# Optimization experiments

Measured on AMD Instinct MI355X. Metric: run time of the kernel, lower is better.

The kernel has to match this reference:

```python
import jax, jax.numpy as jnp
import numpy as np

NUM_PITCHES = 88
H_FEAT = 188
LSTM_UNITS = 48
N_STATES = 5
CTX_HID = 16
CTX_OUT = 4


def _glorot(key, shape):
    fan_in, fan_out = shape[1], shape[0]
    lim = (6.0 / (fan_in + fan_out)) ** 0.5
    return jax.random.uniform(key, shape, jnp.float32, -lim, lim)


def setup_inputs() -> dict:
    key = jax.random.key(0)
    ks = jax.random.split(key, 16)
    B, T = 16, 256
    pitch_features = jax.random.normal(ks[0], (B, NUM_PITCHES, H_FEAT, T), jnp.float32)
    prev_context = jax.random.uniform(ks[1], (B, NUM_PITCHES, 3), jnp.float32)
    # context net params
    fc1_w = _glorot(ks[2], (CTX_HID, 3)); fc1_b = jnp.zeros((CTX_HID,), jnp.float32)
    fc2_w = _glorot(ks[3], (CTX_HID, CTX_HID)); fc2_b = jnp.zeros((CTX_HID,), jnp.float32)
    fc3_w = _glorot(ks[4], (CTX_OUT, CTX_HID)); fc3_b = jnp.zeros((CTX_OUT,), jnp.float32)
    # lstm1: input H_FEAT+4 -> 48; gates order i,f,g,o (torch convention)
    in1 = H_FEAT + CTX_OUT
    lstm1_wih = _glorot(ks[5], (4 * LSTM_UNITS, in1))
    lstm1_whh = _glorot(ks[6], (4 * LSTM_UNITS, LSTM_UNITS))
    lstm1_bih = jnp.zeros((4 * LSTM_UNITS,), jnp.float32)
    lstm1_bhh = jnp.zeros((4 * LSTM_UNITS,), jnp.float32)
    lstm2_wih = _glorot(ks[7], (4 * LSTM_UNITS, LSTM_UNITS))
    lstm2_whh = _glorot(ks[8], (4 * LSTM_UNITS, LSTM_UNITS))
    lstm2_bih = jnp.zeros((4 * LSTM_UNITS,), jnp.float32)
    lstm2_bhh = jnp.zeros((4 * LSTM_UNITS,), jnp.float32)
    fc_states_w = _glorot(ks[9], (N_STATES, LSTM_UNITS))
    fc_states_b = jnp.zeros((N_STATES,), jnp.float32)
    return dict(pitch_features=pitch_features, prev_context=prev_context,
                fc1_w=fc1_w, fc1_b=fc1_b, fc2_w=fc2_w, fc2_b=fc2_b,
                fc3_w=fc3_w, fc3_b=fc3_b,
                lstm1_wih=lstm1_wih, lstm1_whh=lstm1_whh, lstm1_bih=lstm1_bih, lstm1_bhh=lstm1_bhh,
                lstm2_wih=lstm2_wih, lstm2_whh=lstm2_whh, lstm2_bih=lstm2_bih, lstm2_bhh=lstm2_bhh,
                fc_states_w=fc_states_w, fc_states_b=fc_states_b)


def _lstm_scan(x, wih, whh, bih, bhh):
    # x: (S, N, In); zero init state; returns (S, N, U)
    S, N, _ = x.shape
    U = whh.shape[1]
    xg = jnp.einsum('sni,gi->sng', x, wih) + bih + bhh  # precompute input gates

    def step(carry, xg_t):
        h, c = carry
        g = xg_t + h @ whh.T  # (N, 4U)
        i, f, gg, o = jnp.split(g, 4, axis=-1)
        c = jax.nn.sigmoid(f) * c + jax.nn.sigmoid(i) * jnp.tanh(gg)
        h = jax.nn.sigmoid(o) * jnp.tanh(c)
        return (h, c), h

    init = (jnp.zeros((N, U), x.dtype), jnp.zeros((N, U), x.dtype))
    _, hs = jax.lax.scan(step, init, xg)
    return hs


def reference(pitch_features, prev_context,
              fc1_w, fc1_b, fc2_w, fc2_b, fc3_w, fc3_b,
              lstm1_wih, lstm1_whh, lstm1_bih, lstm1_bhh,
              lstm2_wih, lstm2_whh, lstm2_bih, lstm2_bhh,
              fc_states_w, fc_states_b):
    B, P, H, T = pitch_features.shape
    # Context net (context never updates across t in the original loop)
    x = jax.nn.relu(prev_context @ fc1_w.T + fc1_b)
    x = jax.nn.relu(x @ fc2_w.T + fc2_b)
    ctx_emb = x @ fc3_w.T + fc3_b  # (B, P, 4)
    # Each timestep t is independent: LSTM runs over the pitch axis (len 88)
    # with zero initial state every step. Fold (B, T) into batch N.
    pf = jnp.transpose(pitch_features, (1, 0, 3, 2)).reshape(P, B * T, H)  # (P, BT, H)
    ce = jnp.broadcast_to(ctx_emb[:, None, :, :], (B, T, P, CTX_OUT))
    ce = jnp.transpose(ce, (2, 0, 1, 3)).reshape(P, B * T, CTX_OUT)
    seq = jnp.concatenate([pf, ce], axis=-1)  # (P, BT, H+4)
    h = _lstm_scan(seq, lstm1_wih, lstm1_whh, lstm1_bih, lstm1_bhh)
    h = _lstm_scan(h, lstm2_wih, lstm2_whh, lstm2_bih, lstm2_bhh)
    logits = h @ fc_states_w.T + fc_states_b  # (P, BT, 5)
    logits = logits.reshape(P, B, T, N_STATES)
    logits = jnp.transpose(logits, (1, 0, 3, 2))  # (B, P, 5, T)
    return jax.nn.softmax(logits, axis=2)
```

## Files before the change

### kernel.cpp

```cpp
#include <hip/hip_runtime.h>
#include <hip/hip_bf16.h>
#include <cstdint>

#define P_ 88
#define B_ 16
#define T_ 256
#define H_ 188
#define G_ 192
#define U_ 48
#define N_ 4096

typedef __attribute__((ext_vector_type(8))) short bf16x8;
typedef __attribute__((ext_vector_type(8))) _Float16 f16x8;
typedef __attribute__((ext_vector_type(4))) float f32x4;

__device__ __forceinline__ float sigf(float x) {
  return __builtin_amdgcn_rcpf(1.0f + __expf(-x));
}
__device__ __forceinline__ float tanh_f(float x) {
  return 1.0f - 2.0f * __builtin_amdgcn_rcpf(1.0f + __expf(2.0f * x));
}
__device__ __forceinline__ unsigned short f2bs(float v) {
  union { __hip_bfloat16 h; unsigned short s; } u;
  u.h = __float2bfloat16(v);
  return u.s;
}
__device__ __forceinline__ float bs2f(unsigned short s) {
  union { unsigned int u; float f; } x;
  x.u = ((unsigned int)s) << 16;
  return x.f;
}
__device__ __forceinline__ float hs2f(unsigned short s) {
  union { unsigned short u; _Float16 h; } x;
  x.u = s;
  return (float)x.h;
}
__device__ __forceinline__ unsigned short f2hs(float v) {
  union { _Float16 h; unsigned short s; } x;
  x.h = (_Float16)v;
  return x.s;
}

__global__ void ctx_kernel(const float* __restrict__ pc,
                           const float* __restrict__ fc1w, const float* __restrict__ fc1b,
                           const float* __restrict__ fc2w, const float* __restrict__ fc2b,
                           const float* __restrict__ fc3w, const float* __restrict__ fc3b,
                           const float* __restrict__ wih1,
                           const float* __restrict__ bih1, const float* __restrict__ bhh1,
                           float* __restrict__ ctxg) {
  int bp = blockIdx.x * 64 + threadIdx.x;
  if (bp >= B_ * P_) return;
  float p0 = pc[bp * 3 + 0], p1 = pc[bp * 3 + 1], p2 = pc[bp * 3 + 2];
  float x1[16], x2[16];
#pragma unroll
  for (int jj = 0; jj < 16; ++jj)
    x1[jj] = fmaxf(0.f, fc1w[jj * 3 + 0] * p0 + fc1w[jj * 3 + 1] * p1 + fc1w[jj * 3 + 2] * p2 + fc1b[jj]);
#pragma unroll
  for (int jj = 0; jj < 16; ++jj) {
    float s = fc2b[jj];
#pragma unroll
    for (int i = 0; i < 16; ++i) s += fc2w[jj * 16 + i] * x1[i];
    x2[jj] = fmaxf(0.f, s);
  }
  float ce[4];
#pragma unroll
  for (int jj = 0; jj < 4; ++jj) {
    float s = fc3b[jj];
#pragma unroll
    for (int i = 0; i < 16; ++i) s += fc3w[jj * 16 + i] * x2[i];
    ce[jj] = s;
  }
  float* op = ctxg + (size_t)bp * G_;
  for (int g = 0; g < G_; ++g) {
    const float* wr = wih1 + (size_t)g * G_ + H_;
    op[g] = bih1[g] + bhh1[g] + ce[0] * wr[0] + ce[1] * wr[1] + ce[2] * wr[2] + ce[3] * wr[3];
  }
}

__global__ __launch_bounds__(256) void wfrag_kernel(const float* __restrict__ wih1,
                                                    f16x8* __restrict__ wfrag) {
  const int idx = blockIdx.x * 256 + threadIdx.x;
  if (idx >= 12 * 6 * 64) return;
  const int l = idx & 63;
  const int kc = (idx >> 6) % 6;
  const int j = idx / 384;
  const int g = j * 16 + (l & 15);
  const int k0 = kc * 32 + (l >> 4) * 8;
  f16x8 v;
#pragma unroll
  for (int e = 0; e < 8; ++e) {
    const int k = k0 + e;
    const float wv = (k < H_) ? wih1[(size_t)g * G_ + k] : 0.f;
    v[e] = (_Float16)wv;
  }
  wfrag[idx] = v;
}

__global__ __launch_bounds__(256, 3) void gemm_mfma(const float* __restrict__ pf,
                                                    const f16x8* __restrict__ wfrag,
                                                    const float* __restrict__ ctxg,
                                                    unsigned short* __restrict__ xg2) {
  const int bp = blockIdx.x >> 1, tb = blockIdx.x & 1;
  const int p = bp % P_, b = bp / P_;
  const int tid = threadIdx.x;
  const int w = tid >> 6, l = tid & 63;
  const int lj = l & 15, lq = l >> 4;

  __shared__ __align__(16) char ldsraw[49152];
  _Float16(*Ahi)[34] = (_Float16(*)[34])ldsraw;
  _Float16(*Alo)[34] = (_Float16(*)[34])(ldsraw + 8704);

  float cg[12];
#pragma unroll
  for (int jn = 0; jn < 12; ++jn)
    cg[jn] = ctxg[(size_t)bp * G_ + jn * 16 + lj];

  f32x4 acc[2][12];
#pragma unroll
  for (int mt = 0; mt < 2; ++mt)
#pragma unroll
    for (int jn = 0; jn < 12; ++jn)
#pragma unroll
      for (int r = 0; r < 4; ++r) acc[mt][jn][r] = 0.f;

  const float* Ab = pf + (size_t)bp * H_ * T_ + tb * 128;
  const int kl = tid >> 5;
  const int t4 = (tid & 31) * 4;

  for (int kc = 0; kc < 6; ++kc) {
    __syncthreads();
#pragma unroll
    for (int rr = 0; rr < 4; ++rr) {
      const int kk = rr * 8 + kl;
      const int kg = kc * 32 + kk;
      float a0 = 0.f, a1 = 0.f, a2 = 0.f, a3 = 0.f;
      if (kg < H_) {
        const float4 v = *(const float4*)(Ab + (size_t)kg * T_ + t4);
        a0 = v.x; a1 = v.y; a2 = v.z; a3 = v.w;
      }
      const _Float16 h0 = (_Float16)a0, h1 = (_Float16)a1;
      const _Float16 h2 = (_Float16)a2, h3 = (_Float16)a3;
      Ahi[t4 + 0][kk] = h0; Alo[t4 + 0][kk] = (_Float16)(a0 - (float)h0);
      Ahi[t4 + 1][kk] = h1; Alo[t4 + 1][kk] = (_Float16)(a1 - (float)h1);
      Ahi[t4 + 2][kk] = h2; Alo[t4 + 2][kk] = (_Float16)(a2 - (float)h2);
      Ahi[t4 + 3][kk] = h3; Alo[t4 + 3][kk] = (_Float16)(a3 - (float)h3);
    }
    __syncthreads();
    const int trow = w * 32;
    const f16x8 ahi0 = *(const f16x8*)&Ahi[trow + lj][lq * 8];
    const f16x8 ahi1 = *(const f16x8*)&Ahi[trow + 16 + lj][lq * 8];
    const f16x8 alo0 = *(const f16x8*)&Alo[trow + lj][lq * 8];
    const f16x8 alo1 = *(const f16x8*)&Alo[trow + 16 + lj][lq * 8];
#pragma unroll
    for (int jn = 0; jn < 12; ++jn) {
      const f16x8 wf = wfrag[(jn * 6 + kc) * 64 + l];
      acc[0][jn] = __builtin_amdgcn_mfma_f32_16x16x32_f16(ahi0, wf, acc[0][jn], 0, 0, 0);
      acc[1][jn] = __builtin_amdgcn_mfma_f32_16x16x32_f16(ahi1, wf, acc[1][jn], 0, 0, 0);
      acc[0][jn] = __builtin_amdgcn_mfma_f32_16x16x32_f16(alo0, wf, acc[0][jn], 0, 0, 0);
      acc[1][jn] = __builtin_amdgcn_mfma_f32_16x16x32_f16(alo1, wf, acc[1][jn], 0, 0, 0);
    }
  }
  __syncthreads();

  unsigned short* Cst = (unsigned short*)ldsraw + w * 6144;
#pragma unroll
  for (int mt = 0; mt < 2; ++mt)
#pragma unroll
    for (int jn = 0; jn < 12; ++jn)
#pragma unroll
      for (int r = 0; r < 4; ++r)
        Cst[mt * 3072 + jn * 256 + r * 64 + l] = f2hs(acc[mt][jn][r] + cg[jn]);
  const int nb0 = b * 16 + tb * 8 + w * 2;
  unsigned short* gb = xg2 + ((size_t)p * 256 + nb0) * 3072;
#pragma unroll
  for (int rr = 0; rr < 12; ++rr) {
    const uint4 v = *(const uint4*)(Cst + rr * 512 + l * 8);
    *(uint4*)(gb + rr * 512 + l * 8) = v;
  }
}

__global__ __launch_bounds__(256, 2) void scan_mfma(
    const unsigned short* __restrict__ xg2,
    const float* __restrict__ whh1, const float* __restrict__ wih2,
    const float* __restrict__ whh2, const float* __restrict__ bih2,
    const float* __restrict__ bhh2, const float* __restrict__ fcw,
    const float* __restrict__ fcb, float* __restrict__ out) {
  __shared__ __align__(16) short hh[16][104];
  __shared__ __align__(16) short hl[16][104];
  __shared__ __align__(16) float gs[8][196];
  __shared__ __align__(16) float h2f[8][52];
  __shared__ __align__(16) float fcws[5 * 48];
  __shared__ float logit_s[5][8];
  __shared__ float prob_s[5][8];

  const int tid = threadIdx.x;
  const int w = tid >> 6;
  const int l = tid & 63;
  const int lj = l & 15;
  const int lq = l >> 4;
  const int grp = blockIdx.x >> 1;
  const int half = blockIdx.x & 1;
  const int n0 = blockIdx.x * 8;
  const int b = n0 >> 8, t0 = n0 & 255;

  bf16x8 b1[3][2];
  bf16x8 b2f[3][3];
  float bias2r[3];
#pragma unroll
  for (int i = 0; i < 3; ++i) {
    const int j = w * 48 + i * 16 + lj;
    bias2r[i] = bih2[j] + bhh2[j];
#pragma unroll
    for (int kc = 0; kc < 2; ++kc)
#pragma unroll
      for (int e = 0; e < 8; ++e) {
        const int u = kc * 32 + lq * 8 + e;
        b1[i][kc][e] = (u < U_) ? (short)f2bs(whh1[j * U_ + u]) : (short)0;
      }
#pragma unroll
    for (int kc = 0; kc < 3; ++kc)
#pragma unroll
      for (int e = 0; e < 8; ++e) {
        const int u = kc * 32 + lq * 8 + e;
        b2f[i][kc][e] = (u < U_) ? (short)f2bs(wih2[j * U_ + u])
                                 : (short)f2bs(whh2[j * U_ + (u - U_)]);
      }
  }

  for (int e = tid; e < 16 * 104 / 2; e += 256) {
    ((unsigned int*)hh)[e] = 0u;
    ((unsigned int*)hl)[e] = 0u;
  }
  for (int e = tid; e < 5 * U_; e += 256) fcws[e] = fcw[e];

  const int tn0 = tid / U_, tu0 = tid % U_;
  const int tn1 = (256 + tid) / U_, tu1 = (256 + tid) % U_;
  float c1r[2] = {0.f, 0.f}, c2r[2] = {0.f, 0.f};
  const bool fcth = tid < 40;
  const int fk = tid >> 3, fn = tid & 7;
  const float fcbr = fcth ? fcb[fk] : 0.f;
  const int sk = (tid - 96) >> 3, sn = (tid - 96) & 7;

  unsigned short xp[12];
  {
    const size_t pb = (size_t)grp * 3072;
#pragma unroll
    for (int i = 0; i < 3; ++i)
#pragma unroll
      for (int r = 0; r < 4; ++r)
        xp[i * 4 + r] = (lq < 2)
            ? xg2[pb + (size_t)((w * 3 + i) * 256 + r * 64 + (half * 2 + lq) * 16 + lj)]
            : (unsigned short)0;
  }
  const short* hhrow = &hh[lj][0];
  const short* hlrow = &hl[lj][0];
  __syncthreads();

  for (int p = 0; p < P_; ++p) {
    f32x4 c1f[3];
#pragma unroll
    for (int i = 0; i < 3; ++i)
#pragma unroll
      for (int r = 0; r < 4; ++r) c1f[i][r] = hs2f(xp[i * 4 + r]);
    {
      bf16x8 ah0 = *(const bf16x8*)(hhrow + lq * 8);
      bf16x8 ah1 = *(const bf16x8*)(hhrow + 32 + lq * 8);
      bf16x8 al0 = *(const bf16x8*)(hlrow + lq * 8);
      bf16x8 al1 = *(const bf16x8*)(hlrow + 32 + lq * 8);
#pragma unroll
      for (int i = 0; i < 3; ++i)
        c1f[i] = __builtin_amdgcn_mfma_f32_16x16x32_bf16(ah0, b1[i][0], c1f[i], 0, 0, 0);
#pragma unroll
      for (int i = 0; i < 3; ++i)
        c1f[i] = __builtin_amdgcn_mfma_f32_16x16x32_bf16(ah1, b1[i][1], c1f[i], 0, 0, 0);
#pragma unroll
      for (int i = 0; i < 3; ++i)
        c1f[i] = __builtin_amdgcn_mfma_f32_16x16x32_bf16(al0, b1[i][0], c1f[i], 0, 0, 0);
#pragma unroll
      for (int i = 0; i < 3; ++i)
        c1f[i] = __builtin_amdgcn_mfma_f32_16x16x32_bf16(al1, b1[i][1], c1f[i], 0, 0, 0);
    }
    if (lq < 2) {
#pragma unroll
      for (int i = 0; i < 3; ++i)
#pragma unroll
        for (int r = 0; r < 4; ++r)
          gs[lq * 4 + r][w * 48 + i * 16 + lj] = c1f[i][r];
    }
    if (p > 0 && fcth) {
      float a = fcbr;
#pragma unroll
      for (int uq = 0; uq < 12; ++uq) {
        f32x4 hv = *(const f32x4*)&h2f[fn][uq * 4];
        f32x4 wv = *(const f32x4*)&fcws[fk * 48 + uq * 4];
        a += hv[0] * wv[0] + hv[1] * wv[1] + hv[2] * wv[2] + hv[3] * wv[3];
      }
      logit_s[fk][fn] = a;
    }
    __syncthreads();
    {
      const int n = tn0, u = tu0;
      const float ig = gs[n][u], fg = gs[n][48 + u];
      const float gg = gs[n][96 + u], og = gs[n][144 + u];
      const float cc = sigf(fg) * c1r[0] + sigf(ig) * tanh_f(gg);
      c1r[0] = cc;
      const float h = sigf(og) * tanh_f(cc);
      const unsigned short hb = f2bs(h);
      hh[n][u] = (short)hb;
      hl[n][u] = (short)f2bs(h - bs2f(hb));
    }
    if (tid < 128) {
      const int n = tn1, u = tu1;
      const float ig = gs[n][u], fg = gs[n][48 + u];
      const float gg = gs[n][96 + u], og = gs[n][144 + u];
      const float cc = sigf(fg) * c1r[1] + sigf(ig) * tanh_f(gg);
      c1r[1] = cc;
      const float h = sigf(og) * tanh_f(cc);
      const unsigned short hb = f2bs(h);
      hh[n][u] = (short)hb;
      hl[n][u] = (short)f2bs(h - bs2f(hb));
    }
    if (p > 0 && tid >= 192 && tid < 200) {
      const int n = tid - 192;
      const float l0 = logit_s[0][n], l1 = logit_s[1][n], l2 = logit_s[2][n],
                  l3 = logit_s[3][n], l4 = logit_s[4][n];
      const float m = fmaxf(fmaxf(fmaxf(l0, l1), fmaxf(l2, l3)), l4);
      const float e0 = __expf(l0 - m), e1 = __expf(l1 - m), e2 = __expf(l2 - m),
                  e3 = __expf(l3 - m), e4 = __expf(l4 - m);
      const float rs = __builtin_amdgcn_rcpf(e0 + e1 + e2 + e3 + e4);
      prob_s[0][n] = e0 * rs; prob_s[1][n] = e1 * rs; prob_s[2][n] = e2 * rs;
      prob_s[3][n] = e3 * rs; prob_s[4][n] = e4 * rs;
    }
    __syncthreads();
    if (p < P_ - 1) {
      const size_t pb = (size_t)((p + 1) * 256 + grp) * 3072;
#pragma unroll
      for (int i = 0; i < 3; ++i)
#pragma unroll
        for (int r = 0; r < 4; ++r)
          xp[i * 4 + r] = (lq < 2)
              ? xg2[pb + (size_t)((w * 3 + i) * 256 + r * 64 + (half * 2 + lq) * 16 + lj)]
              : (unsigned short)0;
    }
    f32x4 c2f[3];
#pragma unroll
    for (int i = 0; i < 3; ++i) {
      c2f[i][0] = bias2r[i]; c2f[i][1] = bias2r[i];
      c2f[i][2] = bias2r[i]; c2f[i][3] = bias2r[i];
    }
    {
      bf16x8 a0 = *(const bf16x8*)(hhrow + lq * 8);
      bf16x8 a1 = *(const bf16x8*)(hhrow + 32 + lq * 8);
      bf16x8 a2 = *(const bf16x8*)(hhrow + 64 + lq * 8);
      bf16x8 q0 = *(const bf16x8*)(hlrow + lq * 8);
      bf16x8 q1 = *(const bf16x8*)(hlrow + 32 + lq * 8);
      bf16x8 q2 = *(const bf16x8*)(hlrow + 64 + lq * 8);
#pragma unroll
      for (int i = 0; i < 3; ++i)
        c2f[i] = __builtin_amdgcn_mfma_f32_16x16x32_bf16(a0, b2f[i][0], c2f[i], 0, 0, 0);
#pragma unroll
      for (int i = 0; i < 3; ++i)
        c2f[i] = __builtin_amdgcn_mfma_f32_16x16x32_bf16(a1, b2f[i][1], c2f[i], 0, 0, 0);
#pragma unroll
      for (int i = 0; i < 3; ++i)
        c2f[i] = __builtin_amdgcn_mfma_f32_16x16x32_bf16(a2, b2f[i][2], c2f[i], 0, 0, 0);
#pragma unroll
      for (int i = 0; i < 3; ++i)
        c2f[i] = __builtin_amdgcn_mfma_f32_16x16x32_bf16(q0, b2f[i][0], c2f[i], 0, 0, 0);
#pragma unroll
      for (int i = 0; i < 3; ++i)
        c2f[i] = __builtin_amdgcn_mfma_f32_16x16x32_bf16(q1, b2f[i][1], c2f[i], 0, 0, 0);
#pragma unroll
      for (int i = 0; i < 3; ++i)
        c2f[i] = __builtin_amdgcn_mfma_f32_16x16x32_bf16(q2, b2f[i][2], c2f[i], 0, 0, 0);
    }
    if (lq < 2) {
#pragma unroll
      for (int i = 0; i < 3; ++i)
#pragma unroll
        for (int r = 0; r < 4; ++r)
          gs[lq * 4 + r][w * 48 + i * 16 + lj] = c2f[i][r];
    }
    if (p > 0 && tid >= 96 && tid < 136) {
      out[(((size_t)b * P_ + (p - 1)) * 5 + sk) * T_ + t0 + sn] = prob_s[sk][sn];
    }
    __syncthreads();
    {
      const int n = tn0, u = tu0;
      const float ig = gs[n][u], fg = gs[n][48 + u];
      const float gg = gs[n][96 + u], og = gs[n][144 + u];
      const float cc = sigf(fg) * c2r[0] + sigf(ig) * tanh_f(gg);
      c2r[0] = cc;
      const float h = sigf(og) * tanh_f(cc);
      const unsigned short hb = f2bs(h);
      hh[n][48 + u] = (short)hb;
      hl[n][48 + u] = (short)f2bs(h - bs2f(hb));
      h2f[n][u] = h;
    }
    if (tid < 128) {
      const int n = tn1, u = tu1;
      const float ig = gs[n][u], fg = gs[n][48 + u];
      const float gg = gs[n][96 + u], og = gs[n][144 + u];
      const float cc = sigf(fg) * c2r[1] + sigf(ig) * tanh_f(gg);
      c2r[1] = cc;
      const float h = sigf(og) * tanh_f(cc);
      const unsigned short hb = f2bs(h);
      hh[n][48 + u] = (short)hb;
      hl[n][48 + u] = (short)f2bs(h - bs2f(hb));
      h2f[n][u] = h;
    }
    __syncthreads();
  }
  if (fcth) {
    float a = fcbr;
#pragma unroll
    for (int uq = 0; uq < 12; ++uq) {
      f32x4 hv = *(const f32x4*)&h2f[fn][uq * 4];
      f32x4 wv = *(const f32x4*)&fcws[fk * 48 + uq * 4];
      a += hv[0] * wv[0] + hv[1] * wv[1] + hv[2] * wv[2] + hv[3] * wv[3];
    }
    logit_s[fk][fn] = a;
  }
  __syncthreads();
  if (tid >= 192 && tid < 200) {
    const int n = tid - 192;
    const float l0 = logit_s[0][n], l1 = logit_s[1][n], l2 = logit_s[2][n],
                l3 = logit_s[3][n], l4 = logit_s[4][n];
    const float m = fmaxf(fmaxf(fmaxf(l0, l1), fmaxf(l2, l3)), l4);
    const float e0 = __expf(l0 - m), e1 = __expf(l1 - m), e2 = __expf(l2 - m),
                e3 = __expf(l3 - m), e4 = __expf(l4 - m);
    const float rs = __builtin_amdgcn_rcpf(e0 + e1 + e2 + e3 + e4);
    prob_s[0][n] = e0 * rs; prob_s[1][n] = e1 * rs; prob_s[2][n] = e2 * rs;
    prob_s[3][n] = e3 * rs; prob_s[4][n] = e4 * rs;
  }
  __syncthreads();
  if (tid >= 96 && tid < 136) {
    out[(((size_t)b * P_ + (P_ - 1)) * 5 + sk) * T_ + t0 + sn] = prob_s[sk][sn];
  }
}

extern "C" void kernel_launch(void* const* d_in, const int* in_sizes, int n_in,
                              void* d_out, int out_size, void* d_ws, size_t ws_size,
                              hipStream_t stream) {
  const float* pf   = (const float*)d_in[0];
  const float* pc   = (const float*)d_in[1];
  const float* fc1w = (const float*)d_in[2];
  const float* fc1b = (const float*)d_in[3];
  const float* fc2w = (const float*)d_in[4];
  const float* fc2b = (const float*)d_in[5];
  const float* fc3w = (const float*)d_in[6];
  const float* fc3b = (const float*)d_in[7];
  const float* wih1 = (const float*)d_in[8];
  const float* whh1 = (const float*)d_in[9];
  const float* bih1 = (const float*)d_in[10];
  const float* bhh1 = (const float*)d_in[11];
  const float* wih2 = (const float*)d_in[12];
  const float* whh2 = (const float*)d_in[13];
  const float* bih2 = (const float*)d_in[14];
  const float* bhh2 = (const float*)d_in[15];
  const float* fcw  = (const float*)d_in[16];
  const float* fcb  = (const float*)d_in[17];
  float* out = (float*)d_out;

  char* wsp = (char*)d_ws;
  float* ctxg = (float*)wsp;
  const size_t CTXG_BYTES = (size_t)B_ * P_ * G_ * sizeof(float);
  f16x8* wfrag = (f16x8*)(wsp + CTXG_BYTES);
  const size_t WFRAG_BYTES = (size_t)12 * 6 * 64 * 16;
  unsigned short* xg2 = (unsigned short*)(wsp + CTXG_BYTES + WFRAG_BYTES);

  ctx_kernel<<<22, 64, 0, stream>>>(pc, fc1w, fc1b, fc2w, fc2b, fc3w, fc3b,
                                    wih1, bih1, bhh1, ctxg);
  wfrag_kernel<<<18, 256, 0, stream>>>(wih1, wfrag);
  gemm_mfma<<<B_ * P_ * 2, 256, 0, stream>>>(pf, wfrag, ctxg, xg2);
  scan_mfma<<<N_ / 8, 256, 0, stream>>>(xg2, whh1, wih2, whh2,
                                        bih2, bhh2, fcw, fcb, out);
}
```

Measured before the change: 426.2 us.

## Split MFMA accumulators, prefetch next x-gates earlier, use LDS-only barriers

The recurrent loop now keeps separate accumulators for the high and low bf16 halves of h. This breaks the serial dependency chain between back-to-back MFMAs so they can interleave, and the two halves are summed before the store to LDS. The global prefetch of the next step's input gates moves to the start of the iteration so its latency overlaps the layer-1 MFMAs. __syncthreads is replaced by an inline asm barrier that waits only on lgkmcnt, so in-flight global loads are not drained at each barrier. The risks are higher register pressure and reliance on the compiler to insert the vmcnt wait before xp is used.

```diff
diff --git a/kernel.cpp b/kernel.cpp
--- a/kernel.cpp
+++ b/kernel.cpp
@@ -39,6 +39,10 @@
   union { _Float16 h; unsigned short s; } x;
   x.h = (_Float16)v;
   return x.s;
+}
+
+__device__ __forceinline__ void lds_barrier() {
+  asm volatile("s_waitcnt lgkmcnt(0)\n\ts_barrier" ::: "memory");
 }
 
 __global__ void ctx_kernel(const float* __restrict__ pc,
@@ -254,14 +258,24 @@
   }
   const short* hhrow = &hh[lj][0];
   const short* hlrow = &hl[lj][0];
-  __syncthreads();
+  lds_barrier();
 
   for (int p = 0; p < P_; ++p) {
-    f32x4 c1f[3];
+    f32x4 cH[3], cL[3];
 #pragma unroll
     for (int i = 0; i < 3; ++i)
 #pragma unroll
-      for (int r = 0; r < 4; ++r) c1f[i][r] = hs2f(xp[i * 4 + r]);
+      for (int r = 0; r < 4; ++r) { cH[i][r] = hs2f(xp[i * 4 + r]); cL[i][r] = 0.f; }
+    if (p < P_ - 1) {
+      const size_t pb = (size_t)((p + 1) * 256 + grp) * 3072;
+#pragma unroll
+      for (int i = 0; i < 3; ++i)
+#pragma unroll
+        for (int r = 0; r < 4; ++r)
+          xp[i * 4 + r] = (lq < 2)
+              ? xg2[pb + (size_t)((w * 3 + i) * 256 + r * 64 + (half * 2 + lq) * 16 + lj)]
+              : (unsigned short)0;
+    }
     {
       bf16x8 ah0 = *(const bf16x8*)(hhrow + lq * 8);
       bf16x8 ah1 = *(const bf16x8*)(hhrow + 32 + lq * 8);
@@ -269,23 +283,23 @@
       bf16x8 al1 = *(const bf16x8*)(hlrow + 32 + lq * 8);
 #pragma unroll
       for (int i = 0; i < 3; ++i)
-        c1f[i] = __builtin_amdgcn_mfma_f32_16x16x32_bf16(ah0, b1[i][0], c1f[i], 0, 0, 0);
-#pragma unroll
-      for (int i = 0; i < 3; ++i)
-        c1f[i] = __builtin_amdgcn_mfma_f32_16x16x32_bf16(ah1, b1[i][1], c1f[i], 0, 0, 0);
-#pragma unroll
-      for (int i = 0; i < 3; ++i)
-        c1f[i] = __builtin_amdgcn_mfma_f32_16x16x32_bf16(al0, b1[i][0], c1f[i], 0, 0, 0);
-#pragma unroll
-      for (int i = 0; i < 3; ++i)
-        c1f[i] = __builtin_amdgcn_mfma_f32_16x16x32_bf16(al1, b1[i][1], c1f[i], 0, 0, 0);
+        cH[i] = __builtin_amdgcn_mfma_f32_16x16x32_bf16(ah0, b1[i][0], cH[i], 0, 0, 0);
+#pragma unroll
+      for (int i = 0; i < 3; ++i)
+        cL[i] = __builtin_amdgcn_mfma_f32_16x16x32_bf16(al0, b1[i][0], cL[i], 0, 0, 0);
+#pragma unroll
+      for (int i = 0; i < 3; ++i)
+        cH[i] = __builtin_amdgcn_mfma_f32_16x16x32_bf16(ah1, b1[i][1], cH[i], 0, 0, 0);
+#pragma unroll
+      for (int i = 0; i < 3; ++i)
+        cL[i] = __builtin_amdgcn_mfma_f32_16x16x32_bf16(al1, b1[i][1], cL[i], 0, 0, 0);
     }
     if (lq < 2) {
 #pragma unroll
       for (int i = 0; i < 3; ++i)
 #pragma unroll
         for (int r = 0; r < 4; ++r)
-          gs[lq * 4 + r][w * 48 + i * 16 + lj] = c1f[i][r];
+          gs[lq * 4 + r][w * 48 + i * 16 + lj] = cH[i][r] + cL[i][r];
     }
     if (p > 0 && fcth) {
       float a = fcbr;
@@ -297,7 +311,7 @@
       }
       logit_s[fk][fn] = a;
     }
-    __syncthreads();
+    lds_barrier();
     {
       const int n = tn0, u = tu0;
       const float ig = gs[n][u], fg = gs[n][48 + u];
@@ -331,22 +345,13 @@
       prob_s[0][n] = e0 * rs; prob_s[1][n] = e1 * rs; prob_s[2][n] = e2 * rs;
       prob_s[3][n] = e3 * rs; prob_s[4][n] = e4 * rs;
     }
-    __syncthreads();
-    if (p < P_ - 1) {
-      const size_t pb = (size_t)((p + 1) * 256 + grp) * 3072;
-#pragma unroll
-      for (int i = 0; i < 3; ++i)
-#pragma unroll
-        for (int r = 0; r < 4; ++r)
-          xp[i * 4 + r] = (lq < 2)
-              ? xg2[pb + (size_t)((w * 3 + i) * 256 + r * 64 + (half * 2 + lq) * 16 + lj)]
-              : (unsigned short)0;
-    }
-    f32x4 c2f[3];
+    lds_barrier();
+    f32x4 c2H[3], c2L[3];
 #pragma unroll
     for (int i = 0; i < 3; ++i) {
-      c2f[i][0] = bias2r[i]; c2f[i][1] = bias2r[i];
-      c2f[i][2] = bias2r[i]; c2f[i][3] = bias2r[i];
+      c2H[i][0] = bias2r[i]; c2H[i][1] = bias2r[i];
+      c2H[i][2] = bias2r[i]; c2H[i][3] = bias2r[i];
+      c2L[i][0] = 0.f; c2L[i][1] = 0.f; c2L[i][2] = 0.f; c2L[i][3] = 0.f;
     }
     {
       bf16x8 a0 = *(const bf16x8*)(hhrow + lq * 8);
@@ -357,34 +362,34 @@
       bf16x8 q2 = *(const bf16x8*)(hlrow + 64 + lq * 8);
 #pragma unroll
       for (int i = 0; i < 3; ++i)
-        c2f[i] = __builtin_amdgcn_mfma_f32_16x16x32_bf16(a0, b2f[i][0], c2f[i], 0, 0, 0);
-#pragma unroll
-      for (int i = 0; i < 3; ++i)
-        c2f[i] = __builtin_amdgcn_mfma_f32_16x16x32_bf16(a1, b2f[i][1], c2f[i], 0, 0, 0);
-#pragma unroll
-      for (int i = 0; i < 3; ++i)
-        c2f[i] = __builtin_amdgcn_mfma_f32_16x16x32_bf16(a2, b2f[i][2], c2f[i], 0, 0, 0);
-#pragma unroll
-      for (int i = 0; i < 3; ++i)
-        c2f[i] = __builtin_amdgcn_mfma_f32_16x16x32_bf16(q0, b2f[i][0], c2f[i], 0, 0, 0);
-#pragma unroll
-      for (int i = 0; i < 3; ++i)
-        c2f[i] = __builtin_amdgcn_mfma_f32_16x16x32_bf16(q1, b2f[i][1], c2f[i], 0, 0, 0);
-#pragma unroll
-      for (int i = 0; i < 3; ++i)
-        c2f[i] = __builtin_amdgcn_mfma_f32_16x16x32_bf16(q2, b2f[i][2], c2f[i], 0, 0, 0);
+        c2H[i] = __builtin_amdgcn_mfma_f32_16x16x32_bf16(a0, b2f[i][0], c2H[i], 0, 0, 0);
+#pragma unroll
+      for (int i = 0; i < 3; ++i)
+        c2L[i] = __builtin_amdgcn_mfma_f32_16x16x32_bf16(q0, b2f[i][0], c2L[i], 0, 0, 0);
+#pragma unroll
+      for (int i = 0; i < 3; ++i)
+        c2H[i] = __builtin_amdgcn_mfma_f32_16x16x32_bf16(a1, b2f[i][1], c2H[i], 0, 0, 0);
+#pragma unroll
+      for (int i = 0; i < 3; ++i)
+        c2L[i] = __builtin_amdgcn_mfma_f32_16x16x32_bf16(q1, b2f[i][1], c2L[i], 0, 0, 0);
+#pragma unroll
+      for (int i = 0; i < 3; ++i)
+        c2H[i] = __builtin_amdgcn_mfma_f32_16x16x32_bf16(a2, b2f[i][2], c2H[i], 0, 0, 0);
+#pragma unroll
+      for (int i = 0; i < 3; ++i)
+        c2L[i] = __builtin_amdgcn_mfma_f32_16x16x32_bf16(q2, b2f[i][2], c2L[i], 0, 0, 0);
     }
     if (lq < 2) {
 #pragma unroll
       for (int i = 0; i < 3; ++i)
 #pragma unroll
         for (int r = 0; r < 4; ++r)
-          gs[lq * 4 + r][w * 48 + i * 16 + lj] = c2f[i][r];
+          gs[lq * 4 + r][w * 48 + i * 16 + lj] = c2H[i][r] + c2L[i][r];
     }
     if (p > 0 && tid >= 96 && tid < 136) {
       out[(((size_t)b * P_ + (p - 1)) * 5 + sk) * T_ + t0 + sn] = prob_s[sk][sn];
     }
-    __syncthreads();
+    lds_barrier();
     {
       const int n = tn0, u = tu0;
       const float ig = gs[n][u], fg = gs[n][48 + u];
@@ -409,7 +414,7 @@
       hl[n][48 + u] = (short)f2bs(h - bs2f(hb));
       h2f[n][u] = h;
     }
-    __syncthreads();
+    lds_barrier();
   }
   if (fcth) {
     float a = fcbr;
@@ -421,7 +426,7 @@
     }
     logit_s[fk][fn] = a;
   }
-  __syncthreads();
+  lds_barrier();
   if (tid >= 192 && tid < 200) {
     const int n = tid - 192;
     const float l0 = logit_s[0][n], l1 = logit_s[1][n], l2 = logit_s[2][n],
@@ -433,7 +438,7 @@
     prob_s[0][n] = e0 * rs; prob_s[1][n] = e1 * rs; prob_s[2][n] = e2 * rs;
     prob_s[3][n] = e3 * rs; prob_s[4][n] = e4 * rs;
   }
-  __syncthreads();
+  lds_barrier();
   if (tid >= 96 && tid < 136) {
     out[(((size_t)b * P_ + (P_ - 1)) * 5 + sk) * T_ + t0 + sn] = prob_s[sk][sn];
   }
```

New measurement: 413.2 us. 3.0% less time.
